# Performance work log

Measured on AMD Instinct MI355X. Metric: run time of the kernel, lower is better.

The kernel has to match this reference:

```python
import jax, jax.numpy as jnp
import numpy as np

D_MODEL = 2048
N_HEAD = 16
B, T = 2, 2048
D_HEAD = D_MODEL // N_HEAD          # 128
D_Q = D_MODEL // 3                  # 682
D_KV = D_MODEL // 2                 # 1024
D_QK_N = D_HEAD // 2                # 64
D_QK_R = D_HEAD // 2                # 64
LN_EPS = 1e-5


def setup_inputs() -> dict:
    key = jax.random.key(0)
    ks = jax.random.split(key, 8)
    s = 0.02
    return {
        'x': jax.random.normal(ks[0], (B, T, D_MODEL), dtype=jnp.float32),
        'Wdq_w': jax.random.normal(ks[1], (D_Q, D_MODEL), dtype=jnp.float32) * s,
        'Wdq_b': jnp.zeros((D_Q,), jnp.float32),
        'qn_g': jnp.ones((D_Q,), jnp.float32),
        'qn_b': jnp.zeros((D_Q,), jnp.float32),
        'Wuq_w': jax.random.normal(ks[2], (D_MODEL, D_Q), dtype=jnp.float32) * s,
        'Wuq_b': jnp.zeros((D_MODEL,), jnp.float32),
        'Wdkv_w': jax.random.normal(ks[3], (D_KV + D_QK_R, D_MODEL), dtype=jnp.float32) * s,
        'Wdkv_b': jnp.zeros((D_KV + D_QK_R,), jnp.float32),
        'kvn_g': jnp.ones((D_KV,), jnp.float32),
        'kvn_b': jnp.zeros((D_KV,), jnp.float32),
        'Wukv_w': jax.random.normal(ks[4], (D_MODEL + N_HEAD * D_QK_N, D_KV), dtype=jnp.float32) * s,
        'Wukv_b': jnp.zeros((D_MODEL + N_HEAD * D_QK_N,), jnp.float32),
        'Wo_w': jax.random.normal(ks[5], (D_MODEL, D_MODEL), dtype=jnp.float32) * s,
        'Wo_b': jnp.zeros((D_MODEL,), jnp.float32),
    }


def _linear(x, w, b):
    return jnp.einsum('...i,oi->...o', x, w) + b


def _layernorm(x, g, b):
    mu = jnp.mean(x, axis=-1, keepdims=True)
    var = jnp.mean(jnp.square(x - mu), axis=-1, keepdims=True)
    return (x - mu) * jax.lax.rsqrt(var + LN_EPS) * g + b


def _rotary(x):
    # Faithful to source: positions are taken from axis 1 of x (B, A, T, d)
    A, d = x.shape[1], x.shape[-1]
    inv_freq = (1.0 / 10000.0) ** (jnp.arange(0, d, 2, dtype=jnp.float32) / d)
    freqs = jnp.arange(A, dtype=jnp.float32)[:, None] * inv_freq[None, :]
    cos = jnp.cos(freqs)[None, :, None, :]
    sin = jnp.sin(freqs)[None, :, None, :]
    x1, x2 = jnp.split(x, 2, axis=-1)
    return jnp.concatenate([x1 * cos + x2 * sin, -x1 * sin + x2 * cos], axis=-1)


def reference(x, Wdq_w, Wdq_b, qn_g, qn_b, Wuq_w, Wuq_b,
              Wdkv_w, Wdkv_b, kvn_g, kvn_b, Wukv_w, Wukv_b, Wo_w, Wo_b):
    Bx, Tx, C = x.shape
    # Q path: down-proj -> norm -> up-proj
    c_q = _layernorm(_linear(x, Wdq_w, Wdq_b), qn_g, qn_b)
    q = _linear(c_q, Wuq_w, Wuq_b).reshape(Bx, Tx, N_HEAD, D_HEAD).transpose(0, 2, 1, 3)
    q_n, q_r = q[..., :D_QK_N], q[..., D_QK_N:]
    q_r = _rotary(q_r)
    # KV path
    c_kv = _linear(x, Wdkv_w, Wdkv_b)
    kv_n, k_r = c_kv[..., :D_KV], c_kv[..., D_KV:]
    kv_n = _layernorm(kv_n, kvn_g, kvn_b)
    kv = _linear(kv_n, Wukv_w, Wukv_b).reshape(Bx, Tx, N_HEAD, D_HEAD + D_QK_N).transpose(0, 2, 1, 3)
    k_n, v = kv[..., :D_QK_N], kv[..., D_QK_N:]
    k_r = k_r.reshape(Bx, Tx, 1, D_QK_R).transpose(0, 2, 1, 3)  # (B,1,T,dr)
    k_r = _rotary(k_r)  # identity here (single position), kept for fidelity
    k_r = jnp.broadcast_to(k_r, (Bx, N_HEAD, Tx, D_QK_R))
    q_full = jnp.concatenate([q_n, q_r], axis=-1)   # (B,H,T,d_head)
    k_full = jnp.concatenate([k_n, k_r], axis=-1)   # (B,H,T,d_head)
    # causal SDPA (scale = 1/sqrt(q dim))
    scale = 1.0 / np.sqrt(D_HEAD)
    scores = jnp.einsum('bhqd,bhkd->bhqk', q_full, k_full) * scale
    causal = jnp.tril(jnp.ones((Tx, Tx), dtype=bool))
    scores = jnp.where(causal[None, None], scores, jnp.finfo(scores.dtype).min)
    p = jax.nn.softmax(scores, axis=-1)
    y = jnp.einsum('bhqk,bhkd->bhqd', p, v)
    y = y.transpose(0, 2, 1, 3).reshape(Bx, Tx, C)
    return _linear(y, Wo_w, Wo_b)
```

## Files before the change

### kernel.cpp

```cpp
#include <hip/hip_runtime.h>
#include <math.h>

#define TOK 4096
#define DM 2048
#define DQ 682
#define DQP 704
#define DKV 1024
#define DUKV 3072
#define NH 16
#define T_SEQ 2048
#define NQKV 1792

typedef __attribute__((ext_vector_type(8))) short short8;
typedef __attribute__((ext_vector_type(4))) float floatx4;
typedef __attribute__((ext_vector_type(2))) unsigned int uint2v;

__device__ __forceinline__ unsigned short f2bf(float f) {
  union { float f; unsigned int u; } v; v.f = f;
  unsigned int u = v.u;
  u += 0x7fffu + ((u >> 16) & 1u);
  return (unsigned short)(u >> 16);
}
__device__ __forceinline__ unsigned short f2bf_fast(float f) {
  union { float f; unsigned int u; } v; v.f = f;
  return (unsigned short)((v.u + 0x8000u) >> 16);
}

typedef __attribute__((address_space(1))) const unsigned int as1_u32;
typedef __attribute__((address_space(3))) unsigned int as3_u32;
__device__ __forceinline__ void async16(const void* g, void* l) {
  __builtin_amdgcn_global_load_lds((as1_u32*)g, (as3_u32*)l, 16, 0, 0);
}

__global__ __launch_bounds__(256) void gemm_bf16(
    const unsigned short* __restrict__ A, int lda,
    const unsigned short* __restrict__ B, int ldb,
    const float* __restrict__ bias, float* __restrict__ C, int ldc,
    int Nvalid, int K)
{
  __shared__ __align__(16) unsigned short As[128 * 32];
  __shared__ __align__(16) unsigned short Bs[128 * 32];
  const int tid = threadIdx.x;
  const int w = tid >> 6;
  const int lane = tid & 63;
  const int q = lane >> 4;
  const int r = lane & 15;
  const int bm = blockIdx.y * 128;
  const int bn = blockIdx.x * 128;

  floatx4 acc[4][4];
#pragma unroll
  for (int i = 0; i < 4; i++)
#pragma unroll
    for (int j = 0; j < 4; j++) acc[i][j] = (floatx4){0.f, 0.f, 0.f, 0.f};

  const int srow = tid >> 2;
  const int scol = (tid & 3) * 8;
  const unsigned short* Ag0 = A + (size_t)(bm + srow) * lda + scol;
  const unsigned short* Ag1 = A + (size_t)(bm + 64 + srow) * lda + scol;
  const unsigned short* Bg0 = B + (size_t)(bn + srow) * ldb + scol;
  const unsigned short* Bg1 = B + (size_t)(bn + 64 + srow) * ldb + scol;
  unsigned short* AsL0 = &As[w * 512];
  unsigned short* AsL1 = &As[2048 + w * 512];
  unsigned short* BsL0 = &Bs[w * 512];
  unsigned short* BsL1 = &Bs[2048 + w * 512];

  const int mrow0 = (w >> 1) * 64;
  const int ncol0 = (w & 1) * 64;

  for (int k0 = 0; k0 < K; k0 += 32) {
    async16(Ag0 + k0, AsL0);
    async16(Ag1 + k0, AsL1);
    async16(Bg0 + k0, BsL0);
    async16(Bg1 + k0, BsL1);
    __syncthreads();
    short8 a[4], b[4];
#pragma unroll
    for (int i = 0; i < 4; i++)
      a[i] = *(const short8*)&As[(mrow0 + i * 16 + r) * 32 + q * 8];
#pragma unroll
    for (int j = 0; j < 4; j++)
      b[j] = *(const short8*)&Bs[(ncol0 + j * 16 + r) * 32 + q * 8];
#pragma unroll
    for (int i = 0; i < 4; i++)
#pragma unroll
      for (int j = 0; j < 4; j++)
        acc[i][j] = __builtin_amdgcn_mfma_f32_16x16x32_bf16(a[i], b[j], acc[i][j], 0, 0, 0);
    __syncthreads();
  }

#pragma unroll
  for (int j = 0; j < 4; j++) {
    int gc = bn + ncol0 + j * 16 + r;
    if (gc >= Nvalid) continue;
    float bv = bias[gc];
#pragma unroll
    for (int i = 0; i < 4; i++) {
#pragma unroll
      for (int v = 0; v < 4; v++) {
        int gr = bm + mrow0 + i * 16 + q * 4 + v;
        C[(size_t)gr * ldc + gc] = acc[i][j][v] + bv;
      }
    }
  }
}

__global__ __launch_bounds__(256) void gemm_bf16_obf(
    const unsigned short* __restrict__ A, int lda,
    const unsigned short* __restrict__ B, int ldb,
    const float* __restrict__ bias, unsigned short* __restrict__ C, int ldc,
    int Nvalid, int K)
{
  __shared__ __align__(16) unsigned short As[128 * 32];
  __shared__ __align__(16) unsigned short Bs[128 * 32];
  const int tid = threadIdx.x;
  const int w = tid >> 6;
  const int lane = tid & 63;
  const int q = lane >> 4;
  const int r = lane & 15;
  const int bm = blockIdx.y * 128;
  const int bn = blockIdx.x * 128;

  floatx4 acc[4][4];
#pragma unroll
  for (int i = 0; i < 4; i++)
#pragma unroll
    for (int j = 0; j < 4; j++) acc[i][j] = (floatx4){0.f, 0.f, 0.f, 0.f};

  const int srow = tid >> 2;
  const int scol = (tid & 3) * 8;
  const unsigned short* Ag0 = A + (size_t)(bm + srow) * lda + scol;
  const unsigned short* Ag1 = A + (size_t)(bm + 64 + srow) * lda + scol;
  const unsigned short* Bg0 = B + (size_t)(bn + srow) * ldb + scol;
  const unsigned short* Bg1 = B + (size_t)(bn + 64 + srow) * ldb + scol;
  unsigned short* AsL0 = &As[w * 512];
  unsigned short* AsL1 = &As[2048 + w * 512];
  unsigned short* BsL0 = &Bs[w * 512];
  unsigned short* BsL1 = &Bs[2048 + w * 512];

  const int mrow0 = (w >> 1) * 64;
  const int ncol0 = (w & 1) * 64;

  for (int k0 = 0; k0 < K; k0 += 32) {
    async16(Ag0 + k0, AsL0);
    async16(Ag1 + k0, AsL1);
    async16(Bg0 + k0, BsL0);
    async16(Bg1 + k0, BsL1);
    __syncthreads();
    short8 a[4], b[4];
#pragma unroll
    for (int i = 0; i < 4; i++)
      a[i] = *(const short8*)&As[(mrow0 + i * 16 + r) * 32 + q * 8];
#pragma unroll
    for (int j = 0; j < 4; j++)
      b[j] = *(const short8*)&Bs[(ncol0 + j * 16 + r) * 32 + q * 8];
#pragma unroll
    for (int i = 0; i < 4; i++)
#pragma unroll
      for (int j = 0; j < 4; j++)
        acc[i][j] = __builtin_amdgcn_mfma_f32_16x16x32_bf16(a[i], b[j], acc[i][j], 0, 0, 0);
    __syncthreads();
  }

#pragma unroll
  for (int j = 0; j < 4; j++) {
    int gc = bn + ncol0 + j * 16 + r;
    if (gc >= Nvalid) continue;
    float bv = bias[gc];
#pragma unroll
    for (int i = 0; i < 4; i++) {
#pragma unroll
      for (int v = 0; v < 4; v++) {
        int gr = bm + mrow0 + i * 16 + q * 4 + v;
        C[(size_t)gr * ldc + gc] = f2bf(acc[i][j][v] + bv);
      }
    }
  }
}

__global__ __launch_bounds__(256) void gemm_qrope(
    const unsigned short* __restrict__ A, int lda,
    const unsigned short* __restrict__ B, int ldb,
    const float* __restrict__ bias, unsigned short* __restrict__ Qall, int K)
{
  __shared__ __align__(16) unsigned short As[128 * 32];
  __shared__ __align__(16) unsigned short Bs[128 * 32];
  const int tid = threadIdx.x;
  const int w = tid >> 6;
  const int lane = tid & 63;
  const int q = lane >> 4;
  const int r = lane & 15;
  const int bm = blockIdx.y * 128;
  const int bn = blockIdx.x * 128;
  const int h = blockIdx.x;

  floatx4 acc[4][4];
#pragma unroll
  for (int i = 0; i < 4; i++)
#pragma unroll
    for (int j = 0; j < 4; j++) acc[i][j] = (floatx4){0.f, 0.f, 0.f, 0.f};

  const int srow = tid >> 2;
  const int scol = (tid & 3) * 8;
  const unsigned short* Ag0 = A + (size_t)(bm + srow) * lda + scol;
  const unsigned short* Ag1 = A + (size_t)(bm + 64 + srow) * lda + scol;
  const unsigned short* Bg0 = B + (size_t)(bn + srow) * ldb + scol;
  const unsigned short* Bg1 = B + (size_t)(bn + 64 + srow) * ldb + scol;
  unsigned short* AsL0 = &As[w * 512];
  unsigned short* AsL1 = &As[2048 + w * 512];
  unsigned short* BsL0 = &Bs[w * 512];
  unsigned short* BsL1 = &Bs[2048 + w * 512];

  const int mrow0 = (w >> 1) * 64;
  const int ncol0 = (w & 1) * 64;

  for (int k0 = 0; k0 < K; k0 += 32) {
    async16(Ag0 + k0, AsL0);
    async16(Ag1 + k0, AsL1);
    async16(Bg0 + k0, BsL0);
    async16(Bg1 + k0, BsL1);
    __syncthreads();
    short8 a[4], b[4];
#pragma unroll
    for (int i = 0; i < 4; i++)
      a[i] = *(const short8*)&As[(mrow0 + i * 16 + r) * 32 + q * 8];
#pragma unroll
    for (int j = 0; j < 4; j++)
      b[j] = *(const short8*)&Bs[(ncol0 + j * 16 + r) * 32 + q * 8];
#pragma unroll
    for (int i = 0; i < 4; i++)
#pragma unroll
      for (int j = 0; j < 4; j++)
        acc[i][j] = __builtin_amdgcn_mfma_f32_16x16x32_bf16(a[i], b[j], acc[i][j], 0, 0, 0);
    __syncthreads();
  }

  const float QS = (float)(0.08838834764831845 * 1.4426950408889634);
  if ((w & 1) == 0) {
#pragma unroll
    for (int j = 0; j < 4; j++) {
      int d = j * 16 + r;
      float bv = bias[h * 128 + d];
#pragma unroll
      for (int i = 0; i < 4; i++) {
#pragma unroll
        for (int v = 0; v < 4; v++) {
          int gr = bm + mrow0 + i * 16 + q * 4 + v;
          int bb = gr >> 11, t = gr & 2047;
          Qall[(((size_t)(bb * NH + h)) * T_SEQ + t) * 128 + d] =
              f2bf((acc[i][j][v] + bv) * QS);
        }
      }
    }
  } else {
    float cs[2], sn[2], bv1[2], bv2[2];
#pragma unroll
    for (int jp = 0; jp < 2; jp++) {
      int jj = jp * 16 + r;
      float ang = (float)h * exp2f(-(float)jj * (13.287712379549449f / 32.0f));
      cs[jp] = cosf(ang); sn[jp] = sinf(ang);
      bv1[jp] = bias[h * 128 + 64 + jj];
      bv2[jp] = bias[h * 128 + 96 + jj];
    }
#pragma unroll
    for (int i = 0; i < 4; i++) {
#pragma unroll
      for (int v = 0; v < 4; v++) {
        int gr = bm + mrow0 + i * 16 + q * 4 + v;
        int bb = gr >> 11, t = gr & 2047;
        unsigned short* Qr = Qall + (((size_t)(bb * NH + h)) * T_SEQ + t) * 128;
#pragma unroll
        for (int jp = 0; jp < 2; jp++) {
          int jj = jp * 16 + r;
          float x1 = acc[i][jp][v] + bv1[jp];
          float x2 = acc[i][jp + 2][v] + bv2[jp];
          Qr[64 + jj] = f2bf((x1 * cs[jp] + x2 * sn[jp]) * QS);
          Qr[96 + jj] = f2bf((x2 * cs[jp] - x1 * sn[jp]) * QS);
        }
      }
    }
  }
}

__global__ __launch_bounds__(256) void cvt_bf16_pad(
    const float* __restrict__ in, unsigned short* __restrict__ out,
    int irows, int icols, int ocols, long total)
{
  long idx = (long)blockIdx.x * 256 + threadIdx.x;
  if (idx >= total) return;
  int rr = (int)(idx / ocols);
  int cc = (int)(idx - (long)rr * ocols);
  out[idx] = (rr < irows && cc < icols) ? f2bf(in[(size_t)rr * icols + cc]) : 0;
}

__global__ __launch_bounds__(256) void bias_concat(
    const float* __restrict__ a, const float* __restrict__ b,
    float* __restrict__ out)
{
  int i = blockIdx.x * 256 + threadIdx.x;
  if (i >= NQKV) return;
  out[i] = (i < DQ) ? a[i] : ((i < DQP) ? 0.f : b[i - DQP]);
}

__device__ __forceinline__ float block_sum(float v, float* sbuf) {
#pragma unroll
  for (int off = 32; off > 0; off >>= 1) v += __shfl_down(v, off, 64);
  int wid = threadIdx.x >> 6;
  __syncthreads();
  if ((threadIdx.x & 63) == 0) sbuf[wid] = v;
  __syncthreads();
  return sbuf[0] + sbuf[1] + sbuf[2] + sbuf[3];
}

__global__ __launch_bounds__(256) void ln_bf16_kernel(
    const float* __restrict__ in, int istride,
    unsigned short* __restrict__ out, int ocols,
    const float* __restrict__ g, const float* __restrict__ bta, int D)
{
  __shared__ float sbuf[4];
  size_t row = blockIdx.x;
  const float* xr = in + row * istride;
  float s = 0.f;
  for (int i = threadIdx.x; i < D; i += 256) s += xr[i];
  float mu = block_sum(s, sbuf) / (float)D;
  float v = 0.f;
  for (int i = threadIdx.x; i < D; i += 256) { float d = xr[i] - mu; v += d * d; }
  float var = block_sum(v, sbuf) / (float)D;
  float rstd = rsqrtf(var + 1e-5f);
  unsigned short* orow = out + row * ocols;
  for (int i = threadIdx.x; i < ocols; i += 256)
    orow[i] = (i < D) ? f2bf((xr[i] - mu) * rstd * g[i] + bta[i]) : 0;
}

__global__ __launch_bounds__(256) void repack_k_blk(
    const unsigned short* __restrict__ kv_bf, const float* __restrict__ cqkv,
    unsigned short* __restrict__ K)
{
  int idx = blockIdx.x * 256 + threadIdx.x;
  int dlow = idx & 31;
  int tt   = (idx >> 5) & 63;
  int dhi  = (idx >> 11) & 3;
  int kt   = (idx >> 13) & 31;
  int bh   = idx >> 18;
  int d = dhi * 32 + dlow;
  int t = kt * 64 + tt;
  int b = bh >> 4, h = bh & 15;
  unsigned short val;
  if (d < 64)
    val = kv_bf[((size_t)(b * T_SEQ + t)) * DUKV + h * 192 + d];
  else
    val = f2bf(cqkv[((size_t)(b * T_SEQ + t)) * NQKV + 1728 + (d - 64)]);
  K[idx] = val;
}

__global__ __launch_bounds__(256) void repack_v_blk(
    const unsigned short* __restrict__ kv_bf, unsigned short* __restrict__ V)
{
  __shared__ unsigned short T[64 * 132];
  int kt = blockIdx.x, bh = blockIdx.y;
  int b = bh >> 4, h = bh & 15;
  int tid = threadIdx.x;
#pragma unroll
  for (int p = 0; p < 8; p++) {
    int t = p * 8 + (tid >> 5);
    int dbase = (tid & 31) * 4;
    const unsigned short* src =
        kv_bf + ((size_t)(b * T_SEQ + kt * 64 + t)) * DUKV + h * 192 + 64 + dbase;
    unsigned short v0 = src[0], v1 = src[1], v2 = src[2], v3 = src[3];
    unsigned short* dst = &T[t * 132 + dbase];
    dst[0] = v0; dst[1] = v1; dst[2] = v2; dst[3] = v3;
  }
  __syncthreads();
  unsigned short* out = V + ((size_t)(bh * 32 + kt)) * 8192;
#pragma unroll
  for (int p = 0; p < 4; p++) {
    int o = p * 2048 + tid * 8;
    int c2 = o >> 12;
    int dd = (o >> 5) & 127;
    int tl = o & 31;
    short8 pack;
#pragma unroll
    for (int i = 0; i < 8; i++)
      pack[i] = (short)T[(c2 * 32 + tl + i) * 132 + dd];
    *(short8*)&out[o] = pack;
  }
}

__global__ __launch_bounds__(256, 2) void attn_mfma3(
    const unsigned short* __restrict__ Qall,
    const unsigned short* __restrict__ Kblk,
    const unsigned short* __restrict__ Vblk,
    unsigned short* __restrict__ y)
{
  __shared__ __align__(16) unsigned short sm[37376];
  const int x = (int)blockIdx.x;
  const int b = (int)blockIdx.z;
  const int qt = b ? (15 - x) : x;
  const int h = blockIdx.y;
  const int tid = threadIdx.x;
  const int w = tid >> 6, lane = tid & 63, q = lane >> 4, r = lane & 15;
  const int bh = b * NH + h;

  short8 qb[2][4];
#pragma unroll
  for (int g = 0; g < 2; g++) {
    const unsigned short* Qrow =
        Qall + ((size_t)bh * T_SEQ + (size_t)qt * 128 + w * 32 + g * 16 + r) * 128 + q * 8;
#pragma unroll
    for (int c = 0; c < 4; c++) qb[g][c] = *(const short8*)(Qrow + c * 32);
  }

  floatx4 oacc[2][8];
#pragma unroll
  for (int g = 0; g < 2; g++)
#pragma unroll
    for (int jd = 0; jd < 8; jd++) oacc[g][jd] = (floatx4){0.f, 0.f, 0.f, 0.f};
  float m_i[2] = {-3.0e38f, -3.0e38f}, l_i[2] = {0.f, 0.f};

  const char* Kg0 = (const char*)(Kblk + ((size_t)(bh * 32)) * 8192);
  const char* Vg0 = (const char*)(Vblk + ((size_t)(bh * 32)) * 8192);
  char* smB = (char*)sm;
  unsigned short* Psw = sm + 32768 + w * 1152;
  const int ktmax = 2 * qt + 1;

#pragma unroll
  for (int i = 0; i < 4; i++) {
    async16(Kg0 + i * 4096 + w * 1024 + lane * 16, smB + i * 4096 + w * 1024);
    async16(Vg0 + i * 4096 + w * 1024 + lane * 16, smB + 32768 + i * 4096 + w * 1024);
  }

  for (int kt = 0; kt <= ktmax; kt++) {
    const int cur = kt & 1;
    __syncthreads();
    if (kt < ktmax) {
      const int nxt = cur ^ 1;
      const char* Kg = Kg0 + (size_t)(kt + 1) * 16384;
      const char* Vg = Vg0 + (size_t)(kt + 1) * 16384;
#pragma unroll
      for (int i = 0; i < 4; i++) {
        async16(Kg + i * 4096 + w * 1024 + lane * 16,
                smB + nxt * 16384 + i * 4096 + w * 1024);
        async16(Vg + i * 4096 + w * 1024 + lane * 16,
                smB + 32768 + nxt * 16384 + i * 4096 + w * 1024);
      }
    }

    const bool activeW = (kt * 64 <= qt * 128 + w * 32 + 31);
    if (activeW) {
      const unsigned short* KsC = sm + cur * 8192;
      const unsigned short* VsC = sm + 16384 + cur * 8192;

      floatx4 sacc[2][4];
#pragma unroll
      for (int g = 0; g < 2; g++)
#pragma unroll
        for (int j = 0; j < 4; j++) sacc[g][j] = (floatx4){0.f, 0.f, 0.f, 0.f};
#pragma unroll
      for (int c = 0; c < 4; c++) {
        short8 ak[4];
#pragma unroll
        for (int j = 0; j < 4; j++)
          ak[j] = *(const short8*)&KsC[c * 2048 + (j * 16 + r) * 32 + q * 8];
#pragma unroll
        for (int g = 0; g < 2; g++)
#pragma unroll
          for (int j = 0; j < 4; j++)
            sacc[g][j] = __builtin_amdgcn_mfma_f32_16x16x32_bf16(ak[j], qb[g][c], sacc[g][j], 0, 0, 0);
      }

#pragma unroll
      for (int g = 0; g < 2; g++) {
        float sv[16];
#pragma unroll
        for (int j = 0; j < 4; j++)
#pragma unroll
          for (int v = 0; v < 4; v++) sv[j * 4 + v] = sacc[g][j][v];
        const int rel = qt * 128 + w * 32 + g * 16 + r - kt * 64;
        if (rel < 63) {
#pragma unroll
          for (int j = 0; j < 4; j++)
#pragma unroll
            for (int v = 0; v < 4; v++)
              if (j * 16 + q * 4 + v > rel) sv[j * 4 + v] = -3.0e38f;
        }
        float rm = sv[0];
#pragma unroll
        for (int t16 = 1; t16 < 16; t16++) rm = fmaxf(rm, sv[t16]);
        rm = fmaxf(rm, __shfl_xor(rm, 16, 64));
        rm = fmaxf(rm, __shfl_xor(rm, 32, 64));
        float mnew = fmaxf(m_i[g], rm);
        float alpha = exp2f(m_i[g] - mnew);
        m_i[g] = mnew;
        float p[16], rsum = 0.f;
#pragma unroll
        for (int t16 = 0; t16 < 16; t16++) { p[t16] = exp2f(sv[t16] - mnew); rsum += p[t16]; }
        rsum += __shfl_xor(rsum, 16, 64);
        rsum += __shfl_xor(rsum, 32, 64);
        l_i[g] = l_i[g] * alpha + rsum;
#pragma unroll
        for (int jd = 0; jd < 8; jd++) {
          oacc[g][jd][0] *= alpha; oacc[g][jd][1] *= alpha;
          oacc[g][jd][2] *= alpha; oacc[g][jd][3] *= alpha;
        }
#pragma unroll
        for (int j = 0; j < 4; j++) {
          unsigned int lo = (unsigned int)f2bf_fast(p[j * 4 + 0]) |
                            ((unsigned int)f2bf_fast(p[j * 4 + 1]) << 16);
          unsigned int hi = (unsigned int)f2bf_fast(p[j * 4 + 2]) |
                            ((unsigned int)f2bf_fast(p[j * 4 + 3]) << 16);
          uint2v pk; pk[0] = lo; pk[1] = hi;
          *(uint2v*)&Psw[r * 72 + j * 16 + q * 4] = pk;
        }
#pragma unroll
        for (int c2 = 0; c2 < 2; c2++) {
          short8 pb = *(const short8*)&Psw[r * 72 + c2 * 32 + q * 8];
#pragma unroll
          for (int jd = 0; jd < 8; jd++) {
            short8 bv = *(const short8*)&VsC[c2 * 4096 + (jd * 16 + r) * 32 + q * 8];
            oacc[g][jd] = __builtin_amdgcn_mfma_f32_16x16x32_bf16(bv, pb, oacc[g][jd], 0, 0, 0);
          }
        }
      }
    }
  }

#pragma unroll
  for (int g = 0; g < 2; g++) {
    float inv = 1.0f / l_i[g];
    unsigned short* yr =
        y + ((size_t)(b * T_SEQ) + (size_t)qt * 128 + w * 32 + g * 16 + r) * DM + h * 128;
#pragma unroll
    for (int jd = 0; jd < 8; jd++) {
      unsigned short o0 = f2bf(oacc[g][jd][0] * inv);
      unsigned short o1 = f2bf(oacc[g][jd][1] * inv);
      unsigned short o2 = f2bf(oacc[g][jd][2] * inv);
      unsigned short o3 = f2bf(oacc[g][jd][3] * inv);
      unsigned int lo = (unsigned int)o0 | ((unsigned int)o1 << 16);
      unsigned int hi = (unsigned int)o2 | ((unsigned int)o3 << 16);
      unsigned int* dst = (unsigned int*)(yr + jd * 16 + q * 4);
      dst[0] = lo; dst[1] = hi;
    }
  }
}

extern "C" void kernel_launch(void* const* d_in, const int* in_sizes, int n_in,
                              void* d_out, int out_size, void* d_ws, size_t ws_size,
                              hipStream_t stream) {
  const float* x      = (const float*)d_in[0];
  const float* Wdq_w  = (const float*)d_in[1];
  const float* Wdq_b  = (const float*)d_in[2];
  const float* qn_g   = (const float*)d_in[3];
  const float* qn_b   = (const float*)d_in[4];
  const float* Wuq_w  = (const float*)d_in[5];
  const float* Wuq_b  = (const float*)d_in[6];
  const float* Wdkv_w = (const float*)d_in[7];
  const float* Wdkv_b = (const float*)d_in[8];
  const float* kvn_g  = (const float*)d_in[9];
  const float* kvn_b  = (const float*)d_in[10];
  const float* Wukv_w = (const float*)d_in[11];
  const float* Wukv_b = (const float*)d_in[12];
  const float* Wo_w   = (const float*)d_in[13];
  const float* Wo_b   = (const float*)d_in[14];
  float* out = (float*)d_out;

  float* ws = (float*)d_ws;
  unsigned short* x_bf    = (unsigned short*)(ws);
  unsigned short* y_bf    = (unsigned short*)(ws);
  unsigned short* Wqkv_bf = (unsigned short*)(ws + 4194304);
  unsigned short* Wuq_bf  = (unsigned short*)(ws + 6029312);
  unsigned short* Wukv_bf = (unsigned short*)(ws + 6750208);
  float* bias_qkv = ws + 8323072;
  float* c_qkv    = ws + 8324864;
  unsigned short* c_q_bf = (unsigned short*)(ws + 15664896);
  unsigned short* kvn_bf = (unsigned short*)(ws + 17106688);
  unsigned short* kv_bf  = (unsigned short*)(ws + 19203840);
  unsigned short* Q_all  = (unsigned short*)(ws + 25495296);
  unsigned short* K_blk  = (unsigned short*)(ws + 29689600);
  unsigned short* V_blk  = (unsigned short*)(ws + 33883904);
  unsigned short* Wo_bf  = (unsigned short*)(ws + 38078208);

  dim3 blk(256);

  cvt_bf16_pad<<<(4096L*2048 + 255) / 256, blk, 0, stream>>>(x, x_bf, 4096, 2048, 2048, 4096L*2048);
  cvt_bf16_pad<<<(704L*2048 + 255) / 256, blk, 0, stream>>>(Wdq_w, Wqkv_bf, 682, 2048, 2048, 704L*2048);
  cvt_bf16_pad<<<(1088L*2048 + 255) / 256, blk, 0, stream>>>(Wdkv_w, Wqkv_bf + 704L*2048, 1088, 2048, 2048, 1088L*2048);
  cvt_bf16_pad<<<(2048L*704 + 255) / 256, blk, 0, stream>>>(Wuq_w, Wuq_bf, 2048, 682, 704, 2048L*704);
  cvt_bf16_pad<<<(3072L*1024 + 255) / 256, blk, 0, stream>>>(Wukv_w, Wukv_bf, 3072, 1024, 1024, 3072L*1024);
  cvt_bf16_pad<<<(2048L*2048 + 255) / 256, blk, 0, stream>>>(Wo_w, Wo_bf, 2048, 2048, 2048, 2048L*2048);
  bias_concat<<<7, blk, 0, stream>>>(Wdq_b, Wdkv_b, bias_qkv);

  gemm_bf16<<<dim3(14, 32), blk, 0, stream>>>(x_bf, 2048, Wqkv_bf, 2048, bias_qkv, c_qkv, NQKV, NQKV, 2048);
  ln_bf16_kernel<<<TOK, blk, 0, stream>>>(c_qkv, NQKV, c_q_bf, DQP, qn_g, qn_b, DQ);
  ln_bf16_kernel<<<TOK, blk, 0, stream>>>(c_qkv + DQP, NQKV, kvn_bf, DKV, kvn_g, kvn_b, DKV);
  gemm_qrope<<<dim3(16, 32), blk, 0, stream>>>(c_q_bf, DQP, Wuq_bf, DQP, Wuq_b, Q_all, DQP);
  gemm_bf16_obf<<<dim3(24, 32), blk, 0, stream>>>(kvn_bf, DKV, Wukv_bf, DKV, Wukv_b, kv_bf, DUKV, DUKV, DKV);
  repack_k_blk<<<(2 * NH * T_SEQ * 128) / 256, blk, 0, stream>>>(kv_bf, c_qkv, K_blk);
  repack_v_blk<<<dim3(32, 32), blk, 0, stream>>>(kv_bf, V_blk);
  attn_mfma3<<<dim3(16, 16, 2), blk, 0, stream>>>(Q_all, K_blk, V_blk, y_bf);
  gemm_bf16<<<dim3(16, 32), blk, 0, stream>>>(y_bf, 2048, Wo_bf, 2048, Wo_b, out, DM, DM, 2048);
}
```

Baseline: 476.7 us.

## Double-buffer GEMM LDS tiles, fuse up-projection GEMMs and weight conversion launches

Adds LDS double buffering to the GEMM kernels: the next K-tile is prefetched asynchronously while the current one is multiplied, and one barrier per iteration is dropped. The Q and KV up-projection GEMMs are merged into a single launch over a combined grid. The five weight conversion kernels and the bias concat are folded into one prep launch. Together these aim to cut load latency stalls and launch overhead, at the cost of twice the shared memory per block, which may lower occupancy.

```diff
diff --git a/kernel.cpp b/kernel.cpp
--- a/kernel.cpp
+++ b/kernel.cpp
@@ -32,14 +32,13 @@
   __builtin_amdgcn_global_load_lds((as1_u32*)g, (as3_u32*)l, 16, 0, 0);
 }
 
-__global__ __launch_bounds__(256) void gemm_bf16(
+__global__ __launch_bounds__(256) void gemm_bf16_db(
     const unsigned short* __restrict__ A, int lda,
     const unsigned short* __restrict__ B, int ldb,
     const float* __restrict__ bias, float* __restrict__ C, int ldc,
     int Nvalid, int K)
 {
-  __shared__ __align__(16) unsigned short As[128 * 32];
-  __shared__ __align__(16) unsigned short Bs[128 * 32];
+  __shared__ __align__(16) unsigned short sm[16384];
   const int tid = threadIdx.x;
   const int w = tid >> 6;
   const int lane = tid & 63;
@@ -60,20 +59,27 @@
   const unsigned short* Ag1 = A + (size_t)(bm + 64 + srow) * lda + scol;
   const unsigned short* Bg0 = B + (size_t)(bn + srow) * ldb + scol;
   const unsigned short* Bg1 = B + (size_t)(bn + 64 + srow) * ldb + scol;
-  unsigned short* AsL0 = &As[w * 512];
-  unsigned short* AsL1 = &As[2048 + w * 512];
-  unsigned short* BsL0 = &Bs[w * 512];
-  unsigned short* BsL1 = &Bs[2048 + w * 512];
 
   const int mrow0 = (w >> 1) * 64;
   const int ncol0 = (w & 1) * 64;
 
+  async16(Ag0, &sm[w * 512]);
+  async16(Ag1, &sm[2048 + w * 512]);
+  async16(Bg0, &sm[8192 + w * 512]);
+  async16(Bg1, &sm[8192 + 2048 + w * 512]);
+
   for (int k0 = 0; k0 < K; k0 += 32) {
-    async16(Ag0 + k0, AsL0);
-    async16(Ag1 + k0, AsL1);
-    async16(Bg0 + k0, BsL0);
-    async16(Bg1 + k0, BsL1);
+    const int cur = (k0 >> 5) & 1;
     __syncthreads();
+    if (k0 + 32 < K) {
+      const int nxt = cur ^ 1;
+      async16(Ag0 + k0 + 32, &sm[nxt * 4096 + w * 512]);
+      async16(Ag1 + k0 + 32, &sm[nxt * 4096 + 2048 + w * 512]);
+      async16(Bg0 + k0 + 32, &sm[8192 + nxt * 4096 + w * 512]);
+      async16(Bg1 + k0 + 32, &sm[8192 + nxt * 4096 + 2048 + w * 512]);
+    }
+    const unsigned short* As = &sm[cur * 4096];
+    const unsigned short* Bs = &sm[8192 + cur * 4096];
     short8 a[4], b[4];
 #pragma unroll
     for (int i = 0; i < 4; i++)
@@ -86,7 +92,6 @@
 #pragma unroll
       for (int j = 0; j < 4; j++)
         acc[i][j] = __builtin_amdgcn_mfma_f32_16x16x32_bf16(a[i], b[j], acc[i][j], 0, 0, 0);
-    __syncthreads();
   }
 
 #pragma unroll
@@ -105,21 +110,25 @@
   }
 }
 
-__global__ __launch_bounds__(256) void gemm_bf16_obf(
-    const unsigned short* __restrict__ A, int lda,
-    const unsigned short* __restrict__ B, int ldb,
-    const float* __restrict__ bias, unsigned short* __restrict__ C, int ldc,
-    int Nvalid, int K)
-{
-  __shared__ __align__(16) unsigned short As[128 * 32];
-  __shared__ __align__(16) unsigned short Bs[128 * 32];
+__global__ __launch_bounds__(256) void gemm_up_fused(
+    const unsigned short* __restrict__ Aq, const unsigned short* __restrict__ Bq,
+    const float* __restrict__ biasq, unsigned short* __restrict__ Qall,
+    const unsigned short* __restrict__ Akv, const unsigned short* __restrict__ Bkv,
+    const float* __restrict__ biaskv, unsigned short* __restrict__ kvout)
+{
+  __shared__ __align__(16) unsigned short sm[16384];
   const int tid = threadIdx.x;
   const int w = tid >> 6;
   const int lane = tid & 63;
   const int q = lane >> 4;
   const int r = lane & 15;
+  const int bx = blockIdx.x;
+  const bool isQ = bx < 16;
+  const int bn = isQ ? bx * 128 : (bx - 16) * 128;
   const int bm = blockIdx.y * 128;
-  const int bn = blockIdx.x * 128;
+  const int K = isQ ? DQP : DKV;
+  const unsigned short* A = isQ ? Aq : Akv;
+  const unsigned short* B = isQ ? Bq : Bkv;
 
   floatx4 acc[4][4];
 #pragma unroll
@@ -129,24 +138,31 @@
 
   const int srow = tid >> 2;
   const int scol = (tid & 3) * 8;
-  const unsigned short* Ag0 = A + (size_t)(bm + srow) * lda + scol;
-  const unsigned short* Ag1 = A + (size_t)(bm + 64 + srow) * lda + scol;
-  const unsigned short* Bg0 = B + (size_t)(bn + srow) * ldb + scol;
-  const unsigned short* Bg1 = B + (size_t)(bn + 64 + srow) * ldb + scol;
-  unsigned short* AsL0 = &As[w * 512];
-  unsigned short* AsL1 = &As[2048 + w * 512];
-  unsigned short* BsL0 = &Bs[w * 512];
-  unsigned short* BsL1 = &Bs[2048 + w * 512];
+  const unsigned short* Ag0 = A + (size_t)(bm + srow) * K + scol;
+  const unsigned short* Ag1 = A + (size_t)(bm + 64 + srow) * K + scol;
+  const unsigned short* Bg0 = B + (size_t)(bn + srow) * K + scol;
+  const unsigned short* Bg1 = B + (size_t)(bn + 64 + srow) * K + scol;
 
   const int mrow0 = (w >> 1) * 64;
   const int ncol0 = (w & 1) * 64;
 
+  async16(Ag0, &sm[w * 512]);
+  async16(Ag1, &sm[2048 + w * 512]);
+  async16(Bg0, &sm[8192 + w * 512]);
+  async16(Bg1, &sm[8192 + 2048 + w * 512]);
+
   for (int k0 = 0; k0 < K; k0 += 32) {
-    async16(Ag0 + k0, AsL0);
-    async16(Ag1 + k0, AsL1);
-    async16(Bg0 + k0, BsL0);
-    async16(Bg1 + k0, BsL1);
+    const int cur = (k0 >> 5) & 1;
     __syncthreads();
+    if (k0 + 32 < K) {
+      const int nxt = cur ^ 1;
+      async16(Ag0 + k0 + 32, &sm[nxt * 4096 + w * 512]);
+      async16(Ag1 + k0 + 32, &sm[nxt * 4096 + 2048 + w * 512]);
+      async16(Bg0 + k0 + 32, &sm[8192 + nxt * 4096 + w * 512]);
+      async16(Bg1 + k0 + 32, &sm[8192 + nxt * 4096 + 2048 + w * 512]);
+    }
+    const unsigned short* As = &sm[cur * 4096];
+    const unsigned short* Bs = &sm[8192 + cur * 4096];
     short8 a[4], b[4];
 #pragma unroll
     for (int i = 0; i < 4; i++)
@@ -159,88 +175,32 @@
 #pragma unroll
       for (int j = 0; j < 4; j++)
         acc[i][j] = __builtin_amdgcn_mfma_f32_16x16x32_bf16(a[i], b[j], acc[i][j], 0, 0, 0);
-    __syncthreads();
-  }
-
-#pragma unroll
-  for (int j = 0; j < 4; j++) {
-    int gc = bn + ncol0 + j * 16 + r;
-    if (gc >= Nvalid) continue;
-    float bv = bias[gc];
-#pragma unroll
-    for (int i = 0; i < 4; i++) {
-#pragma unroll
-      for (int v = 0; v < 4; v++) {
-        int gr = bm + mrow0 + i * 16 + q * 4 + v;
-        C[(size_t)gr * ldc + gc] = f2bf(acc[i][j][v] + bv);
-      }
-    }
-  }
-}
-
-__global__ __launch_bounds__(256) void gemm_qrope(
-    const unsigned short* __restrict__ A, int lda,
-    const unsigned short* __restrict__ B, int ldb,
-    const float* __restrict__ bias, unsigned short* __restrict__ Qall, int K)
-{
-  __shared__ __align__(16) unsigned short As[128 * 32];
-  __shared__ __align__(16) unsigned short Bs[128 * 32];
-  const int tid = threadIdx.x;
-  const int w = tid >> 6;
-  const int lane = tid & 63;
-  const int q = lane >> 4;
-  const int r = lane & 15;
-  const int bm = blockIdx.y * 128;
-  const int bn = blockIdx.x * 128;
-  const int h = blockIdx.x;
-
-  floatx4 acc[4][4];
-#pragma unroll
-  for (int i = 0; i < 4; i++)
-#pragma unroll
-    for (int j = 0; j < 4; j++) acc[i][j] = (floatx4){0.f, 0.f, 0.f, 0.f};
-
-  const int srow = tid >> 2;
-  const int scol = (tid & 3) * 8;
-  const unsigned short* Ag0 = A + (size_t)(bm + srow) * lda + scol;
-  const unsigned short* Ag1 = A + (size_t)(bm + 64 + srow) * lda + scol;
-  const unsigned short* Bg0 = B + (size_t)(bn + srow) * ldb + scol;
-  const unsigned short* Bg1 = B + (size_t)(bn + 64 + srow) * ldb + scol;
-  unsigned short* AsL0 = &As[w * 512];
-  unsigned short* AsL1 = &As[2048 + w * 512];
-  unsigned short* BsL0 = &Bs[w * 512];
-  unsigned short* BsL1 = &Bs[2048 + w * 512];
-
-  const int mrow0 = (w >> 1) * 64;
-  const int ncol0 = (w & 1) * 64;
-
-  for (int k0 = 0; k0 < K; k0 += 32) {
-    async16(Ag0 + k0, AsL0);
-    async16(Ag1 + k0, AsL1);
-    async16(Bg0 + k0, BsL0);
-    async16(Bg1 + k0, BsL1);
-    __syncthreads();
-    short8 a[4], b[4];
-#pragma unroll
-    for (int i = 0; i < 4; i++)
-      a[i] = *(const short8*)&As[(mrow0 + i * 16 + r) * 32 + q * 8];
-#pragma unroll
-    for (int j = 0; j < 4; j++)
-      b[j] = *(const short8*)&Bs[(ncol0 + j * 16 + r) * 32 + q * 8];
-#pragma unroll
-    for (int i = 0; i < 4; i++)
-#pragma unroll
-      for (int j = 0; j < 4; j++)
-        acc[i][j] = __builtin_amdgcn_mfma_f32_16x16x32_bf16(a[i], b[j], acc[i][j], 0, 0, 0);
-    __syncthreads();
-  }
-
+  }
+
+  if (!isQ) {
+#pragma unroll
+    for (int j = 0; j < 4; j++) {
+      int gc = bn + ncol0 + j * 16 + r;
+      float bv = biaskv[gc];
+#pragma unroll
+      for (int i = 0; i < 4; i++) {
+#pragma unroll
+        for (int v = 0; v < 4; v++) {
+          int gr = bm + mrow0 + i * 16 + q * 4 + v;
+          kvout[(size_t)gr * DUKV + gc] = f2bf(acc[i][j][v] + bv);
+        }
+      }
+    }
+    return;
+  }
+
+  const int h = bx;
   const float QS = (float)(0.08838834764831845 * 1.4426950408889634);
   if ((w & 1) == 0) {
 #pragma unroll
     for (int j = 0; j < 4; j++) {
       int d = j * 16 + r;
-      float bv = bias[h * 128 + d];
+      float bv = biasq[h * 128 + d];
 #pragma unroll
       for (int i = 0; i < 4; i++) {
 #pragma unroll
@@ -259,8 +219,8 @@
       int jj = jp * 16 + r;
       float ang = (float)h * exp2f(-(float)jj * (13.287712379549449f / 32.0f));
       cs[jp] = cosf(ang); sn[jp] = sinf(ang);
-      bv1[jp] = bias[h * 128 + 64 + jj];
-      bv2[jp] = bias[h * 128 + 96 + jj];
+      bv1[jp] = biasq[h * 128 + 64 + jj];
+      bv2[jp] = biasq[h * 128 + 96 + jj];
     }
 #pragma unroll
     for (int i = 0; i < 4; i++) {
@@ -293,13 +253,41 @@
   out[idx] = (rr < irows && cc < icols) ? f2bf(in[(size_t)rr * icols + cc]) : 0;
 }
 
-__global__ __launch_bounds__(256) void bias_concat(
-    const float* __restrict__ a, const float* __restrict__ b,
-    float* __restrict__ out)
-{
-  int i = blockIdx.x * 256 + threadIdx.x;
-  if (i >= NQKV) return;
-  out[i] = (i < DQ) ? a[i] : ((i < DQP) ? 0.f : b[i - DQP]);
+__device__ __forceinline__ void cvt_region(
+    const float* __restrict__ in, unsigned short* __restrict__ out,
+    int irows, int icols, int ocols, long idx)
+{
+  int rr = (int)(idx / ocols);
+  int cc = (int)(idx - (long)rr * ocols);
+  out[idx] = (rr < irows && cc < icols) ? f2bf(in[(size_t)rr * icols + cc]) : 0;
+}
+
+__global__ __launch_bounds__(256) void prep_weights(
+    const float* __restrict__ Wdq_w, const float* __restrict__ Wdkv_w,
+    const float* __restrict__ Wuq_w, const float* __restrict__ Wukv_w,
+    const float* __restrict__ Wo_w,
+    const float* __restrict__ Wdq_b, const float* __restrict__ Wdkv_b,
+    unsigned short* __restrict__ Wqkv_bf, unsigned short* __restrict__ Wuq_bf,
+    unsigned short* __restrict__ Wukv_bf, unsigned short* __restrict__ Wo_bf,
+    float* __restrict__ bias_qkv)
+{
+  const long bx = blockIdx.x;
+  if (bx < 5632) {
+    cvt_region(Wdq_w, Wqkv_bf, 682, 2048, 2048, bx * 256 + threadIdx.x);
+  } else if (bx < 14336) {
+    cvt_region(Wdkv_w, Wqkv_bf + 704L * 2048, 1088, 2048, 2048,
+               (bx - 5632) * 256 + threadIdx.x);
+  } else if (bx < 19968) {
+    cvt_region(Wuq_w, Wuq_bf, 2048, 682, 704, (bx - 14336) * 256 + threadIdx.x);
+  } else if (bx < 32256) {
+    cvt_region(Wukv_w, Wukv_bf, 3072, 1024, 1024, (bx - 19968) * 256 + threadIdx.x);
+  } else if (bx < 48640) {
+    cvt_region(Wo_w, Wo_bf, 2048, 2048, 2048, (bx - 32256) * 256 + threadIdx.x);
+  } else {
+    int i = (int)(bx - 48640) * 256 + threadIdx.x;
+    if (i < NQKV)
+      bias_qkv[i] = (i < DQ) ? Wdq_b[i] : ((i < DQP) ? 0.f : Wdkv_b[i - DQP]);
+  }
 }
 
 __device__ __forceinline__ float block_sum(float v, float* sbuf) {
@@ -582,20 +570,17 @@
   dim3 blk(256);
 
   cvt_bf16_pad<<<(4096L*2048 + 255) / 256, blk, 0, stream>>>(x, x_bf, 4096, 2048, 2048, 4096L*2048);
-  cvt_bf16_pad<<<(704L*2048 + 255) / 256, blk, 0, stream>>>(Wdq_w, Wqkv_bf, 682, 2048, 2048, 704L*2048);
-  cvt_bf16_pad<<<(1088L*2048 + 255) / 256, blk, 0, stream>>>(Wdkv_w, Wqkv_bf + 704L*2048, 1088, 2048, 2048, 1088L*2048);
-  cvt_bf16_pad<<<(2048L*704 + 255) / 256, blk, 0, stream>>>(Wuq_w, Wuq_bf, 2048, 682, 704, 2048L*704);
-  cvt_bf16_pad<<<(3072L*1024 + 255) / 256, blk, 0, stream>>>(Wukv_w, Wukv_bf, 3072, 1024, 1024, 3072L*1024);
-  cvt_bf16_pad<<<(2048L*2048 + 255) / 256, blk, 0, stream>>>(Wo_w, Wo_bf, 2048, 2048, 2048, 2048L*2048);
-  bias_concat<<<7, blk, 0, stream>>>(Wdq_b, Wdkv_b, bias_qkv);
-
-  gemm_bf16<<<dim3(14, 32), blk, 0, stream>>>(x_bf, 2048, Wqkv_bf, 2048, bias_qkv, c_qkv, NQKV, NQKV, 2048);
+  prep_weights<<<48647, blk, 0, stream>>>(Wdq_w, Wdkv_w, Wuq_w, Wukv_w, Wo_w,
+                                          Wdq_b, Wdkv_b,
+                                          Wqkv_bf, Wuq_bf, Wukv_bf, Wo_bf, bias_qkv);
+
+  gemm_bf16_db<<<dim3(14, 32), blk, 0, stream>>>(x_bf, 2048, Wqkv_bf, 2048, bias_qkv, c_qkv, NQKV, NQKV, 2048);
   ln_bf16_kernel<<<TOK, blk, 0, stream>>>(c_qkv, NQKV, c_q_bf, DQP, qn_g, qn_b, DQ);
   ln_bf16_kernel<<<TOK, blk, 0, stream>>>(c_qkv + DQP, NQKV, kvn_bf, DKV, kvn_g, kvn_b, DKV);
-  gemm_qrope<<<dim3(16, 32), blk, 0, stream>>>(c_q_bf, DQP, Wuq_bf, DQP, Wuq_b, Q_all, DQP);
-  gemm_bf16_obf<<<dim3(24, 32), blk, 0, stream>>>(kvn_bf, DKV, Wukv_bf, DKV, Wukv_b, kv_bf, DUKV, DUKV, DKV);
+  gemm_up_fused<<<dim3(40, 32), blk, 0, stream>>>(c_q_bf, Wuq_bf, Wuq_b, Q_all,
+                                                  kvn_bf, Wukv_bf, Wukv_b, kv_bf);
   repack_k_blk<<<(2 * NH * T_SEQ * 128) / 256, blk, 0, stream>>>(kv_bf, c_qkv, K_blk);
   repack_v_blk<<<dim3(32, 32), blk, 0, stream>>>(kv_bf, V_blk);
   attn_mfma3<<<dim3(16, 16, 2), blk, 0, stream>>>(Q_all, K_blk, V_blk, y_bf);
-  gemm_bf16<<<dim3(16, 32), blk, 0, stream>>>(y_bf, 2048, Wo_bf, 2048, Wo_b, out, DM, DM, 2048);
-}
+  gemm_bf16_db<<<dim3(16, 32), blk, 0, stream>>>(y_bf, 2048, Wo_bf, 2048, Wo_b, out, DM, DM, 2048);
+}
```

Result: faster. 426.9 us (-10.5%).
